# Kernel optimization log

Measured on AMD Instinct MI355X. Metric: run time of the kernel, lower is better.

The kernel has to match this reference:

```python
import jax, jax.numpy as jnp
import numpy as np

N = 100000   # nodes per graph
E = 1600000  # edges (avg degree 16)
B = 2        # num_graph (batch)
F_IN = 116   # num_input
EMB = 12     # embedding dim
H = 128      # hidden_size


def setup_inputs() -> dict:
    key = jax.random.key(0)
    ks = jax.random.split(key, 8)
    node = jax.random.normal(ks[0], (B, N, F_IN), dtype=jnp.float32)
    node_type = jax.random.randint(ks[1], (N,), 0, 8, dtype=jnp.int32)
    edge_index = jax.random.randint(ks[2], (2, E), 0, N, dtype=jnp.int32)
    embed = jax.random.normal(ks[3], (8, EMB), dtype=jnp.float32)
    d1 = F_IN + EMB
    W1 = jax.random.normal(ks[4], (d1, H), dtype=jnp.float32) / np.sqrt(d1)
    b1 = jnp.zeros((H,), dtype=jnp.float32)
    W2 = jax.random.normal(ks[5], (H, H), dtype=jnp.float32) / np.sqrt(H)
    b2 = jnp.zeros((H,), dtype=jnp.float32)
    return {"node": node, "node_type": node_type, "edge_index": edge_index,
            "embed": embed, "W1": W1, "b1": b1, "W2": W2, "b2": b2}


def _gcn_conv(x, src, dst, W, b):
    """PyG GCNConv: symmetric norm with self-loops, linear (no lin bias), bias after agg.
    x: [B, N, F]; src/dst: [E] int; W: [F, H]; b: [H]."""
    n = x.shape[1]
    # degree over (A + I), computed on destination nodes
    deg = jnp.zeros((n,), x.dtype).at[dst].add(1.0) + 1.0
    dis = jax.lax.rsqrt(deg)  # deg^{-1/2}
    xw = jnp.einsum('bnf,fh->bnh', x, W)          # [B, N, H]
    norm = dis[src] * dis[dst]                    # [E]
    msgs = xw[:, src, :] * norm[None, :, None]    # [B, E, H]
    agg = jax.vmap(lambda m: jax.ops.segment_sum(m, dst, num_segments=n))(msgs)
    agg = agg + xw * (dis * dis)[None, :, None]   # self-loop contribution
    return agg + b


def reference(node, node_type, edge_index, embed, W1, b1, W2, b2):
    src, dst = edge_index[0], edge_index[1]
    emb = embed[node_type]                                      # [N, EMB]
    b = node.shape[0]
    emb_b = jnp.broadcast_to(emb[None], (b,) + emb.shape)       # repeat over batch
    x = jnp.concatenate([node, emb_b], axis=2)                  # [B, N, F_IN+EMB]
    x = jax.nn.relu(_gcn_conv(x, src, dst, W1, b1))
    # F.dropout in eval mode is identity
    x = _gcn_conv(x, src, dst, W2, b2)
    return jnp.mean(x, axis=1)                                  # [B, H]
```

## Files before the change

### kernel.cpp

```cpp
#include <hip/hip_runtime.h>
#include <stdint.h>

typedef unsigned int uint32;
typedef unsigned short ushort16;
typedef __attribute__((ext_vector_type(8))) short bf16x8;
typedef __attribute__((ext_vector_type(4))) float f32x4;
typedef __attribute__((ext_vector_type(2))) float f32x2;

#define F_IN 116
#define HID  128
#define EMBD 12
#define IDXMASK 0x03FFFFFFu
#define BCAP 2048
#define PCAP 2560

__device__ __forceinline__ ushort16 f2bf(float f) {
    uint32 x = __float_as_uint(f);
    uint32 r = (x + 0x7fffu + ((x >> 16) & 1u)) >> 16;
    return (ushort16)r;
}

__global__ void k_init(int* __restrict__ bcurD, int* __restrict__ bcurS,
                       float* __restrict__ partial, uint32* __restrict__ xwzrow, int K) {
    int i = blockIdx.x * 256 + threadIdx.x;
    if (i < K) { bcurD[i] = i * BCAP; bcurS[i] = i * BCAP; }
    if (blockIdx.x == 0) {
        partial[threadIdx.x] = 0.f;
        if (threadIdx.x < 64) xwzrow[threadIdx.x] = 0u;
    }
}

__global__ void k_prepB(const float* __restrict__ W1, ushort16* __restrict__ W1s) {
    int tid = blockIdx.x * blockDim.x + threadIdx.x;
    if (tid >= 2048) return;
    int q = tid & 3, n = (tid >> 2) & 15, t = (tid >> 6) & 7, kc = (tid >> 9) & 3;
    int chunk = ((kc * 8 + t) * 64 + n * 4 + q);
#pragma unroll
    for (int j = 0; j < 8; ++j) {
        int k = kc * 32 + q * 8 + j;
        W1s[chunk * 8 + j] = f2bf(W1[k * HID + t * 16 + n]);
    }
}

__global__ __launch_bounds__(256) void k_bin(
    const int* __restrict__ src, const int* __restrict__ dst,
    int* __restrict__ bcurD, int* __restrict__ bcurS,
    uint32* __restrict__ ebufD, uint32* __restrict__ ebufS, int E) {
    __shared__ int lhD[2048], lbD[2048], lhS[2048], lbS[2048];
    const int tid = threadIdx.x;
    const int e0 = blockIdx.x * 8192;
    const int eend = min(e0 + 8192, E);
    for (int i = tid; i < 2048; i += 256) { lhD[i] = 0; lhS[i] = 0; }
    __syncthreads();
    for (int e = e0 + tid; e < eend; e += 256) {
        atomicAdd(&lhD[dst[e] >> 6], 1);
        atomicAdd(&lhS[src[e] >> 6], 1);
    }
    __syncthreads();
    const int rot = (blockIdx.x * 277) & 2047;
#pragma unroll
    for (int i = 0; i < 8; ++i) {
        int k = (rot + tid + i * 256) & 2047;
        int c = lhD[k]; lbD[k] = c ? atomicAdd(&bcurD[k], c) : 0; lhD[k] = 0;
        int d = lhS[k]; lbS[k] = d ? atomicAdd(&bcurS[k], d) : 0; lhS[k] = 0;
    }
    __syncthreads();
    for (int e = e0 + tid; e < eend; e += 256) {
        int s = src[e], d = dst[e];
        int bkD = d >> 6;
        int p = lbD[bkD] + atomicAdd(&lhD[bkD], 1);
        if (p < (bkD + 1) * BCAP) ebufD[p] = ((uint32)(d & 63) << 26) | (uint32)s;
        int bkS = s >> 6;
        int p2 = lbS[bkS] + atomicAdd(&lhS[bkS], 1);
        if (p2 < (bkS + 1) * BCAP) ebufS[p2] = ((uint32)(s & 63) << 26) | (uint32)d;
    }
}

__global__ __launch_bounds__(256) void k_csr(
    const uint32* __restrict__ ebufD, const int* __restrict__ bcurD,
    int* __restrict__ rowstart, int* __restrict__ rowcnt, float* __restrict__ dis,
    int* __restrict__ csr, int N, int ZROW) {
    __shared__ int cnt[64];
    __shared__ int cur[64];
    __shared__ int lst[64];
    const int b = blockIdx.x, tid = threadIdx.x;
    const int r0 = b * BCAP;
    const int r1 = min(bcurD[b], r0 + BCAP);
    if (tid < 64) cnt[tid] = 0;
    __syncthreads();
    for (int p = r0 + tid; p < r1; p += 256)
        atomicAdd(&cnt[ebufD[p] >> 26], 1);
    __syncthreads();
    if (tid == 0) {
        int run = b * PCAP;
#pragma unroll
        for (int l = 0; l < 64; ++l) { lst[l] = run; run += (cnt[l] + 7) & ~7; }
    }
    __syncthreads();
    if (tid < 64) {
        int n = (b << 6) + tid;
        cur[tid] = lst[tid];
        if (n < N) {
            rowstart[n] = lst[tid];
            rowcnt[n] = ((cnt[tid] + 7) & ~7) >> 3;
            dis[n] = rsqrtf(1.0f + (float)cnt[tid]);
        }
    }
    __syncthreads();
    for (int p = r0 + tid; p < r1; p += 256) {
        uint32 v = ebufD[p];
        int l = v >> 26;
        csr[atomicAdd(&cur[l], 1)] = (int)(v & IDXMASK);
    }
    __syncthreads();
    if (tid < 64) {
        int end = lst[tid] + ((cnt[tid] + 7) & ~7);
        for (int p = cur[tid]; p < end; ++p) csr[p] = ZROW;
    }
}

__global__ __launch_bounds__(256) void k_souts(
    const uint32* __restrict__ ebufS, const int* __restrict__ bcurS,
    const float* __restrict__ dis, float* __restrict__ souts, int N) {
    __shared__ float lso[64];
    const int b = blockIdx.x, tid = threadIdx.x;
    const int r0 = b * BCAP;
    const int r1 = min(bcurS[b], r0 + BCAP);
    if (tid < 64) lso[tid] = 0.f;
    __syncthreads();
    for (int p = r0 + tid; p < r1; p += 256) {
        uint32 v = ebufS[p];
        atomicAdd(&lso[v >> 26], dis[v & IDXMASK]);
    }
    __syncthreads();
    if (tid < 64) {
        int n = (b << 6) + tid;
        if (n < N) souts[n] = lso[tid];
    }
}

__global__ __launch_bounds__(256, 4) void k_gemm(
    const float* __restrict__ node, const ushort16* __restrict__ W1s,
    const int* __restrict__ ntype, const float* __restrict__ embed,
    const float* __restrict__ dis, uint32* __restrict__ xw8, int N, int M)
{
    __shared__ ushort16 ldsA[4 * 4 * 64 * 8];
    __shared__ float ldis[32];
    const int tid = threadIdx.x;
    const int row0 = blockIdx.x * 64;

    if (tid < 32) {
        int n = (row0 >> 1) + tid;
        ldis[tid] = (n < N) ? dis[n] : 0.f;
    }

    const int g = tid & 31;
    const int kc0 = g >> 3, q0 = (g >> 1) & 3, half = g & 1;
#pragma unroll
    for (int j = 0; j < 8; ++j) {
        int r = (tid >> 5) + j * 8;
        int m = row0 + r;
        int n = m >> 1, b = m & 1;
        float4 v = make_float4(0.f, 0.f, 0.f, 0.f);
        if (n < N) {
            if (g < 29) v = *(const float4*)(node + ((size_t)b * N + n) * F_IN + g * 4);
            else        v = *(const float4*)(embed + ntype[n] * EMBD + (g - 29) * 4);
        }
        uint32 u0 = (uint32)f2bf(v.x) | ((uint32)f2bf(v.y) << 16);
        uint32 u1 = (uint32)f2bf(v.z) | ((uint32)f2bf(v.w) << 16);
        int mt = r >> 4, mloc = r & 15;
        int chunk = (mt * 4 + kc0) * 64 + mloc * 4 + q0;
        *(uint2*)&ldsA[chunk * 8 + half * 4] = make_uint2(u0, u1);
    }
    __syncthreads();

    const int lane = tid & 63;
    const int w = tid >> 6;
    const int fragsel = (lane & 15) * 4 + (lane >> 4);

    f32x4 acc[8];
#pragma unroll
    for (int ct = 0; ct < 8; ++ct) acc[ct] = (f32x4){0.f, 0.f, 0.f, 0.f};

#pragma unroll
    for (int kc = 0; kc < 4; ++kc) {
        bf16x8 bfr = *(const bf16x8*)&ldsA[(((w * 4 + kc) * 64) + fragsel) * 8];
#pragma unroll
        for (int ct = 0; ct < 8; ++ct) {
            bf16x8 afr = *(const bf16x8*)&W1s[(((kc * 8 + ct) * 64) + fragsel) * 8];
            acc[ct] = __builtin_amdgcn_mfma_f32_16x16x32_bf16(afr, bfr, acc[ct], 0, 0, 0);
        }
    }

    const int row = lane & 15, q = lane >> 4;
    int m = row0 + w * 16 + row;
    if (m < M) {
        float dn = ldis[(w * 16 + row) >> 1];
        uint32* rowp = xw8 + (size_t)m * 32;
#pragma unroll
        for (int ct = 0; ct < 8; ++ct) {
            f32x4 a = acc[ct];
            int u = __builtin_amdgcn_cvt_pk_fp8_f32(a[0] * dn, a[1] * dn, 0, false);
            u = __builtin_amdgcn_cvt_pk_fp8_f32(a[2] * dn, a[3] * dn, u, true);
            rowp[ct * 4 + q] = (uint32)u;
        }
    }
}

__global__ __launch_bounds__(256) void k_gather(
    const uint32* __restrict__ xw8, const int* __restrict__ csr,
    const int* __restrict__ rowstart, const int* __restrict__ rowcnt,
    const float* __restrict__ dis, const float* __restrict__ souts,
    const float* __restrict__ b1, float* __restrict__ partial, int N)
{
    __shared__ float sm[4][256];
    const int tid  = threadIdx.x;
    const int lane = tid & 63;
    const int wid  = tid >> 6;
    const int wv = (blockIdx.x * blockDim.x + tid) >> 6;
    const int nw = (gridDim.x * blockDim.x) >> 6;
    const int c0 = (lane & 31) * 4;
    const int slot = (lane >> 5) * HID + c0;
    const float bb0 = b1[c0], bb1 = b1[c0 + 1], bb2 = b1[c0 + 2], bb3 = b1[c0 + 3];

    float p0 = 0.f, p1 = 0.f, p2 = 0.f, p3 = 0.f;

    for (int n = wv * 2; n < N; n += nw * 2) {
        const int ns = __builtin_amdgcn_readfirstlane(n);
        const int v2 = (ns + 1 < N);
        const int st1 = rowstart[ns];
        const int c1  = rowcnt[ns];
        const float dn1 = dis[ns], so1 = souts[ns];
        const int st2 = v2 ? rowstart[ns + 1] : 0;
        const int c2  = v2 ? rowcnt[ns + 1] : 0;
        const float dn2 = v2 ? dis[ns + 1] : 0.f;
        const float so2 = v2 ? souts[ns + 1] : 0.f;

        uint32 sv1 = xw8[(size_t)ns * 64 + lane];
        uint32 sv2 = v2 ? xw8[((size_t)ns + 1) * 64 + lane] : 0u;
        f32x2 lo1 = __builtin_amdgcn_cvt_pk_f32_fp8(sv1, false);
        f32x2 hi1 = __builtin_amdgcn_cvt_pk_f32_fp8(sv1, true);
        f32x2 lo2 = __builtin_amdgcn_cvt_pk_f32_fp8(sv2, false);
        f32x2 hi2 = __builtin_amdgcn_cvt_pk_f32_fp8(sv2, true);
        float a10 = lo1.x, a11 = lo1.y, a12 = hi1.x, a13 = hi1.y;
        float a20 = lo2.x, a21 = lo2.y, a22 = hi2.x, a23 = hi2.y;

        const int jm = max(c1, c2);
        for (int j = 0; j < jm; ++j) {
            if (j < c1) {
                int4 ca = *(const int4*)&csr[st1 + j * 8];
                int4 cb = *(const int4*)&csr[st1 + j * 8 + 4];
                uint32 v[8];
                v[0] = xw8[(size_t)ca.x * 64 + lane];
                v[1] = xw8[(size_t)ca.y * 64 + lane];
                v[2] = xw8[(size_t)ca.z * 64 + lane];
                v[3] = xw8[(size_t)ca.w * 64 + lane];
                v[4] = xw8[(size_t)cb.x * 64 + lane];
                v[5] = xw8[(size_t)cb.y * 64 + lane];
                v[6] = xw8[(size_t)cb.z * 64 + lane];
                v[7] = xw8[(size_t)cb.w * 64 + lane];
#pragma unroll
                for (int k = 0; k < 8; ++k) {
                    f32x2 lo = __builtin_amdgcn_cvt_pk_f32_fp8(v[k], false);
                    f32x2 hi = __builtin_amdgcn_cvt_pk_f32_fp8(v[k], true);
                    a10 += lo.x; a11 += lo.y; a12 += hi.x; a13 += hi.y;
                }
            }
            if (j < c2) {
                int4 ca = *(const int4*)&csr[st2 + j * 8];
                int4 cb = *(const int4*)&csr[st2 + j * 8 + 4];
                uint32 v[8];
                v[0] = xw8[(size_t)ca.x * 64 + lane];
                v[1] = xw8[(size_t)ca.y * 64 + lane];
                v[2] = xw8[(size_t)ca.z * 64 + lane];
                v[3] = xw8[(size_t)ca.w * 64 + lane];
                v[4] = xw8[(size_t)cb.x * 64 + lane];
                v[5] = xw8[(size_t)cb.y * 64 + lane];
                v[6] = xw8[(size_t)cb.z * 64 + lane];
                v[7] = xw8[(size_t)cb.w * 64 + lane];
#pragma unroll
                for (int k = 0; k < 8; ++k) {
                    f32x2 lo = __builtin_amdgcn_cvt_pk_f32_fp8(v[k], false);
                    f32x2 hi = __builtin_amdgcn_cvt_pk_f32_fp8(v[k], true);
                    a20 += lo.x; a21 += lo.y; a22 += hi.x; a23 += hi.y;
                }
            }
        }

        float cf1 = dn1 * (dn1 + so1);
        p0 = fmaf(cf1, fmaxf(fmaf(dn1, a10, bb0), 0.f), p0);
        p1 = fmaf(cf1, fmaxf(fmaf(dn1, a11, bb1), 0.f), p1);
        p2 = fmaf(cf1, fmaxf(fmaf(dn1, a12, bb2), 0.f), p2);
        p3 = fmaf(cf1, fmaxf(fmaf(dn1, a13, bb3), 0.f), p3);
        if (v2) {
            float cf2 = dn2 * (dn2 + so2);
            p0 = fmaf(cf2, fmaxf(fmaf(dn2, a20, bb0), 0.f), p0);
            p1 = fmaf(cf2, fmaxf(fmaf(dn2, a21, bb1), 0.f), p1);
            p2 = fmaf(cf2, fmaxf(fmaf(dn2, a22, bb2), 0.f), p2);
            p3 = fmaf(cf2, fmaxf(fmaf(dn2, a23, bb3), 0.f), p3);
        }
    }

    *(float4*)&sm[wid][slot] = make_float4(p0, p1, p2, p3);
    __syncthreads();
    if (tid < 256) {
        float s = sm[0][tid] + sm[1][tid] + sm[2][tid] + sm[3][tid];
        atomicAdd(&partial[tid], s);
    }
}

__global__ void k_final(const float* __restrict__ partial, const float* __restrict__ W2,
                        const float* __restrict__ b2, float* __restrict__ out, float invN) {
    int tid = threadIdx.x;
    int b = tid >> 7, h = tid & 127;
    float acc = 0.f;
#pragma unroll 8
    for (int k = 0; k < HID; ++k)
        acc += partial[b * HID + k] * W2[k * HID + h];
    out[tid] = acc * invN + b2[h];
}

extern "C" void kernel_launch(void* const* d_in, const int* in_sizes, int n_in,
                              void* d_out, int out_size, void* d_ws, size_t ws_size,
                              hipStream_t stream) {
    const float* node  = (const float*)d_in[0];
    const int*   ntype = (const int*)d_in[1];
    const int*   eidx  = (const int*)d_in[2];
    const float* embed = (const float*)d_in[3];
    const float* W1    = (const float*)d_in[4];
    const float* b1    = (const float*)d_in[5];
    const float* W2    = (const float*)d_in[6];
    const float* b2    = (const float*)d_in[7];
    float* out = (float*)d_out;

    const int N  = in_sizes[1];
    const int E  = in_sizes[2] / 2;
    const int B  = in_sizes[0] / (N * F_IN);
    const int M  = B * N;
    const int K  = (N + 63) >> 6;

    const int* src = eidx;
    const int* dst = eidx + E;

    char* ws = (char*)d_ws;
    size_t off = 0;
    auto alloc = [&](size_t bytes) -> void* {
        void* p = ws + off;
        off += (bytes + 255) & ~(size_t)255;
        return p;
    };
    uint32*   xw8     = (uint32*)alloc((size_t)(M + 2) * 128);
    int*      csr     = (int*)alloc((size_t)K * PCAP * sizeof(int));
    uint32*   ebufD   = (uint32*)alloc((size_t)K * BCAP * sizeof(uint32));
    uint32*   ebufS   = (uint32*)alloc((size_t)K * BCAP * sizeof(uint32));
    int*      rowstart= (int*)alloc((size_t)N * sizeof(int));
    int*      rowcnt  = (int*)alloc((size_t)N * sizeof(int));
    float*    dis     = (float*)alloc((size_t)N * sizeof(float));
    float*    souts   = (float*)alloc((size_t)N * sizeof(float));
    ushort16* W1s     = (ushort16*)alloc(4 * 8 * 64 * 8 * sizeof(ushort16));
    int*      bcurD   = (int*)alloc((size_t)K * sizeof(int));
    int*      bcurS   = (int*)alloc((size_t)K * sizeof(int));
    float*    partial = (float*)alloc(2 * HID * sizeof(float));

    k_init<<<(K + 255) / 256, 256, 0, stream>>>(bcurD, bcurS, partial, xw8 + (size_t)N * 64, K);
    k_prepB<<<8, 256, 0, stream>>>(W1, W1s);
    k_bin<<<(E + 8191) / 8192, 256, 0, stream>>>(src, dst, bcurD, bcurS, ebufD, ebufS, E);
    k_csr<<<K, 256, 0, stream>>>(ebufD, bcurD, rowstart, rowcnt, dis, csr, N, N);
    k_souts<<<K, 256, 0, stream>>>(ebufS, bcurS, dis, souts, N);
    k_gemm<<<(M + 63) / 64, 256, 0, stream>>>(node, W1s, ntype, embed, dis, xw8, N, M);
    k_gather<<<2048, 256, 0, stream>>>(xw8, csr, rowstart, rowcnt, dis, souts, b1, partial, N);
    k_final<<<1, 256, 0, stream>>>(partial, W2, b2, out, 1.0f / (float)N);
}
```

Before: 391.6 us.

## Widen edge buckets to 256 nodes and pack per-node metadata into int4

```diff
diff --git a/kernel.cpp b/kernel.cpp
--- a/kernel.cpp
+++ b/kernel.cpp
@@ -10,9 +10,9 @@
 #define F_IN 116
 #define HID  128
 #define EMBD 12
-#define IDXMASK 0x03FFFFFFu
-#define BCAP 2048
-#define PCAP 2560
+#define IDX24 0x00FFFFFFu
+#define BCAP 4608
+#define PCAP 6400
 
 __device__ __forceinline__ ushort16 f2bf(float f) {
     uint32 x = __float_as_uint(f);
@@ -46,97 +46,98 @@
     const int* __restrict__ src, const int* __restrict__ dst,
     int* __restrict__ bcurD, int* __restrict__ bcurS,
     uint32* __restrict__ ebufD, uint32* __restrict__ ebufS, int E) {
-    __shared__ int lhD[2048], lbD[2048], lhS[2048], lbS[2048];
+    __shared__ int lhD[512], lbD[512], lhS[512], lbS[512];
     const int tid = threadIdx.x;
     const int e0 = blockIdx.x * 8192;
     const int eend = min(e0 + 8192, E);
-    for (int i = tid; i < 2048; i += 256) { lhD[i] = 0; lhS[i] = 0; }
+    for (int i = tid; i < 512; i += 256) { lhD[i] = 0; lhS[i] = 0; }
     __syncthreads();
     for (int e = e0 + tid; e < eend; e += 256) {
-        atomicAdd(&lhD[dst[e] >> 6], 1);
-        atomicAdd(&lhS[src[e] >> 6], 1);
-    }
-    __syncthreads();
-    const int rot = (blockIdx.x * 277) & 2047;
-#pragma unroll
-    for (int i = 0; i < 8; ++i) {
-        int k = (rot + tid + i * 256) & 2047;
+        atomicAdd(&lhD[dst[e] >> 8], 1);
+        atomicAdd(&lhS[src[e] >> 8], 1);
+    }
+    __syncthreads();
+    const int rot = (blockIdx.x * 277) & 511;
+#pragma unroll
+    for (int i = 0; i < 2; ++i) {
+        int k = (rot + tid + i * 256) & 511;
         int c = lhD[k]; lbD[k] = c ? atomicAdd(&bcurD[k], c) : 0; lhD[k] = 0;
         int d = lhS[k]; lbS[k] = d ? atomicAdd(&bcurS[k], d) : 0; lhS[k] = 0;
     }
     __syncthreads();
     for (int e = e0 + tid; e < eend; e += 256) {
         int s = src[e], d = dst[e];
-        int bkD = d >> 6;
+        int bkD = d >> 8;
         int p = lbD[bkD] + atomicAdd(&lhD[bkD], 1);
-        if (p < (bkD + 1) * BCAP) ebufD[p] = ((uint32)(d & 63) << 26) | (uint32)s;
-        int bkS = s >> 6;
+        if (p < (bkD + 1) * BCAP) ebufD[p] = ((uint32)(d & 255) << 24) | (uint32)s;
+        int bkS = s >> 8;
         int p2 = lbS[bkS] + atomicAdd(&lhS[bkS], 1);
-        if (p2 < (bkS + 1) * BCAP) ebufS[p2] = ((uint32)(s & 63) << 26) | (uint32)d;
+        if (p2 < (bkS + 1) * BCAP) ebufS[p2] = ((uint32)(s & 255) << 24) | (uint32)d;
     }
 }
 
 __global__ __launch_bounds__(256) void k_csr(
     const uint32* __restrict__ ebufD, const int* __restrict__ bcurD,
-    int* __restrict__ rowstart, int* __restrict__ rowcnt, float* __restrict__ dis,
+    int4* __restrict__ meta, float* __restrict__ dis,
     int* __restrict__ csr, int N, int ZROW) {
-    __shared__ int cnt[64];
-    __shared__ int cur[64];
-    __shared__ int lst[64];
+    __shared__ int cnt[256];
+    __shared__ int cur[256];
+    __shared__ int lst[256];
+    __shared__ int ps[256];
     const int b = blockIdx.x, tid = threadIdx.x;
     const int r0 = b * BCAP;
     const int r1 = min(bcurD[b], r0 + BCAP);
-    if (tid < 64) cnt[tid] = 0;
+    cnt[tid] = 0;
     __syncthreads();
     for (int p = r0 + tid; p < r1; p += 256)
-        atomicAdd(&cnt[ebufD[p] >> 26], 1);
-    __syncthreads();
-    if (tid == 0) {
-        int run = b * PCAP;
-#pragma unroll
-        for (int l = 0; l < 64; ++l) { lst[l] = run; run += (cnt[l] + 7) & ~7; }
-    }
-    __syncthreads();
-    if (tid < 64) {
-        int n = (b << 6) + tid;
-        cur[tid] = lst[tid];
-        if (n < N) {
-            rowstart[n] = lst[tid];
-            rowcnt[n] = ((cnt[tid] + 7) & ~7) >> 3;
-            dis[n] = rsqrtf(1.0f + (float)cnt[tid]);
-        }
+        atomicAdd(&cnt[ebufD[p] >> 24], 1);
+    __syncthreads();
+    const int pl = (cnt[tid] + 7) & ~7;
+    ps[tid] = pl;
+    __syncthreads();
+    for (int off = 1; off < 256; off <<= 1) {
+        int t = (tid >= off) ? ps[tid - off] : 0;
+        __syncthreads();
+        ps[tid] += t;
+        __syncthreads();
+    }
+    const int start = b * PCAP + ps[tid] - pl;
+    lst[tid] = start;
+    cur[tid] = start;
+    const int n = (b << 8) + tid;
+    float dl = rsqrtf(1.0f + (float)cnt[tid]);
+    if (n < N) {
+        dis[n] = dl;
+        meta[n] = make_int4(start, pl >> 3, __float_as_int(dl), 0);
     }
     __syncthreads();
     for (int p = r0 + tid; p < r1; p += 256) {
         uint32 v = ebufD[p];
-        int l = v >> 26;
-        csr[atomicAdd(&cur[l], 1)] = (int)(v & IDXMASK);
-    }
-    __syncthreads();
-    if (tid < 64) {
-        int end = lst[tid] + ((cnt[tid] + 7) & ~7);
+        csr[atomicAdd(&cur[v >> 24], 1)] = (int)(v & IDX24);
+    }
+    __syncthreads();
+    {
+        int end = lst[tid] + pl;
         for (int p = cur[tid]; p < end; ++p) csr[p] = ZROW;
     }
 }
 
 __global__ __launch_bounds__(256) void k_souts(
     const uint32* __restrict__ ebufS, const int* __restrict__ bcurS,
-    const float* __restrict__ dis, float* __restrict__ souts, int N) {
-    __shared__ float lso[64];
+    const float* __restrict__ dis, int4* __restrict__ meta, int N) {
+    __shared__ float lso[256];
     const int b = blockIdx.x, tid = threadIdx.x;
     const int r0 = b * BCAP;
     const int r1 = min(bcurS[b], r0 + BCAP);
-    if (tid < 64) lso[tid] = 0.f;
+    lso[tid] = 0.f;
     __syncthreads();
     for (int p = r0 + tid; p < r1; p += 256) {
         uint32 v = ebufS[p];
-        atomicAdd(&lso[v >> 26], dis[v & IDXMASK]);
-    }
-    __syncthreads();
-    if (tid < 64) {
-        int n = (b << 6) + tid;
-        if (n < N) souts[n] = lso[tid];
-    }
+        atomicAdd(&lso[v >> 24], dis[v & IDX24]);
+    }
+    __syncthreads();
+    int n = (b << 8) + tid;
+    if (n < N) meta[n].w = __float_as_int(lso[tid]);
 }
 
 __global__ __launch_bounds__(256, 4) void k_gemm(
@@ -209,9 +210,8 @@
 
 __global__ __launch_bounds__(256) void k_gather(
     const uint32* __restrict__ xw8, const int* __restrict__ csr,
-    const int* __restrict__ rowstart, const int* __restrict__ rowcnt,
-    const float* __restrict__ dis, const float* __restrict__ souts,
-    const float* __restrict__ b1, float* __restrict__ partial, int N)
+    const int4* __restrict__ meta, const float* __restrict__ b1,
+    float* __restrict__ partial, int N)
 {
     __shared__ float sm[4][256];
     const int tid  = threadIdx.x;
@@ -228,13 +228,12 @@
     for (int n = wv * 2; n < N; n += nw * 2) {
         const int ns = __builtin_amdgcn_readfirstlane(n);
         const int v2 = (ns + 1 < N);
-        const int st1 = rowstart[ns];
-        const int c1  = rowcnt[ns];
-        const float dn1 = dis[ns], so1 = souts[ns];
-        const int st2 = v2 ? rowstart[ns + 1] : 0;
-        const int c2  = v2 ? rowcnt[ns + 1] : 0;
-        const float dn2 = v2 ? dis[ns + 1] : 0.f;
-        const float so2 = v2 ? souts[ns + 1] : 0.f;
+        const int4 m1 = meta[ns];
+        const int4 m2 = v2 ? meta[ns + 1] : make_int4(0, 0, 0, 0);
+        const int st1 = m1.x, c1 = m1.y;
+        const float dn1 = __int_as_float(m1.z), so1 = __int_as_float(m1.w);
+        const int st2 = m2.x, c2 = m2.y;
+        const float dn2 = __int_as_float(m2.z), so2 = __int_as_float(m2.w);
 
         uint32 sv1 = xw8[(size_t)ns * 64 + lane];
         uint32 sv2 = v2 ? xw8[((size_t)ns + 1) * 64 + lane] : 0u;
@@ -337,7 +336,7 @@
     const int E  = in_sizes[2] / 2;
     const int B  = in_sizes[0] / (N * F_IN);
     const int M  = B * N;
-    const int K  = (N + 63) >> 6;
+    const int K  = (N + 255) >> 8;
 
     const int* src = eidx;
     const int* dst = eidx + E;
@@ -353,10 +352,8 @@
     int*      csr     = (int*)alloc((size_t)K * PCAP * sizeof(int));
     uint32*   ebufD   = (uint32*)alloc((size_t)K * BCAP * sizeof(uint32));
     uint32*   ebufS   = (uint32*)alloc((size_t)K * BCAP * sizeof(uint32));
-    int*      rowstart= (int*)alloc((size_t)N * sizeof(int));
-    int*      rowcnt  = (int*)alloc((size_t)N * sizeof(int));
+    int4*     meta    = (int4*)alloc((size_t)N * sizeof(int4));
     float*    dis     = (float*)alloc((size_t)N * sizeof(float));
-    float*    souts   = (float*)alloc((size_t)N * sizeof(float));
     ushort16* W1s     = (ushort16*)alloc(4 * 8 * 64 * 8 * sizeof(ushort16));
     int*      bcurD   = (int*)alloc((size_t)K * sizeof(int));
     int*      bcurS   = (int*)alloc((size_t)K * sizeof(int));
@@ -365,9 +362,9 @@
     k_init<<<(K + 255) / 256, 256, 0, stream>>>(bcurD, bcurS, partial, xw8 + (size_t)N * 64, K);
     k_prepB<<<8, 256, 0, stream>>>(W1, W1s);
     k_bin<<<(E + 8191) / 8192, 256, 0, stream>>>(src, dst, bcurD, bcurS, ebufD, ebufS, E);
-    k_csr<<<K, 256, 0, stream>>>(ebufD, bcurD, rowstart, rowcnt, dis, csr, N, N);
-    k_souts<<<K, 256, 0, stream>>>(ebufS, bcurS, dis, souts, N);
+    k_csr<<<K, 256, 0, stream>>>(ebufD, bcurD, meta, dis, csr, N, N);
+    k_souts<<<K, 256, 0, stream>>>(ebufS, bcurS, dis, meta, N);
     k_gemm<<<(M + 63) / 64, 256, 0, stream>>>(node, W1s, ntype, embed, dis, xw8, N, M);
-    k_gather<<<2048, 256, 0, stream>>>(xw8, csr, rowstart, rowcnt, dis, souts, b1, partial, N);
+    k_gather<<<2048, 256, 0, stream>>>(xw8, csr, meta, b1, partial, N);
     k_final<<<1, 256, 0, stream>>>(partial, W2, b2, out, 1.0f / (float)N);
 }
```

Result: no change. 388.0 us (-0.9%).
